# Kernel tuning notes

Hardware: AMD Instinct MI355X
Metric: run time of the kernel (lower is better)

Reference implementation:

```python
import jax, jax.numpy as jnp
import numpy as np

N, E, D, CAT, BINS, B, NNEG = 50000, 1600000, 128, 768, 100, 4096, 4


def _spmm(row, col, val, x):
    # torch.spmm(adj, x) with adj in COO form: out[r] += val * x[c]
    return jax.ops.segment_sum(val[:, None] * x[col], row, num_segments=N)


def _bn(x, g, b):
    # BatchNorm1d in training mode: biased batch statistics
    m = jnp.mean(x, axis=0)
    v = jnp.var(x, axis=0)
    return (x - m) * jax.lax.rsqrt(v + 1e-5) * g + b


def _two_att(qx, x, Wq1, bq1, Wk1, bk1, Wv1, bv1, Wq2, bq2, Wk2, bk2, Wv2, bv2, Wcat, bcat):
    # qx, x: [b, 2, D]. NOTE: original uses nn.Softmax(dim=1), i.e. softmax over the
    # QUERY axis of the [b, q, k] score matrix -- reproduced faithfully here.
    scale = 1.0 / (D ** 0.5)
    q = qx @ Wq1 + bq1
    k = x @ Wk1 + bk1
    v = x @ Wv1 + bv1
    a = jax.nn.softmax(jnp.einsum('bqd,bkd->bqk', q, k) * scale, axis=1)
    h = jnp.einsum('bqk,bkd->bqd', a, v)
    q = h @ Wq2 + bq2
    k = h @ Wk2 + bk2
    v = h @ Wv2 + bv2
    a = jax.nn.softmax(jnp.einsum('bqd,bkd->bqk', q, k) * scale, axis=1)
    h = jnp.einsum('bqk,bkd->bqd', a, v)
    return jnp.concatenate([h[:, 0], h[:, 1]], axis=1) @ Wcat + bcat


def setup_inputs():
    key = jax.random.key(0)
    ks = jax.random.split(key, 32)
    p = lambda i, shape: jax.random.normal(ks[i], shape, dtype=jnp.float32) * 0.05
    return {
        'features': jax.random.normal(ks[0], (N, 2 * CAT), dtype=jnp.float32),
        'price': jax.random.randint(ks[1], (N,), 0, BINS),
        'adj_row': jax.random.randint(ks[2], (E,), 0, N),
        'adj_col': jax.random.randint(ks[3], (E,), 0, N),
        'adj_val': jax.random.uniform(ks[4], (E,), dtype=jnp.float32),
        'train_set': jax.random.randint(ks[5], (B, 2 + NNEG), 0, N),
        'W_cid2': p(6, (CAT, D)), 'b_cid2': p(7, (D,)),
        'W_cid3': p(8, (CAT, D)), 'b_cid3': p(9, (D,)),
        'price_table': p(10, (BINS, D)),
        'W_emb': p(11, (3 * D, D)), 'b_emb': p(12, (D,)),
        'W_low': p(13, (D, D)), 'W_mid': p(14, (D, D)),
        'bn1_g': jnp.ones((D,), jnp.float32), 'bn1_b': jnp.zeros((D,), jnp.float32),
        'bn2_g': jnp.ones((D,), jnp.float32), 'bn2_b': jnp.zeros((D,), jnp.float32),
        'Wq1': p(15, (D, D)), 'bq1': p(16, (D,)),
        'Wk1': p(17, (D, D)), 'bk1': p(18, (D,)),
        'Wv1': p(19, (D, D)), 'bv1': p(20, (D,)),
        'Wq2': p(21, (D, D)), 'bq2': p(22, (D,)),
        'Wk2': p(23, (D, D)), 'bk2': p(24, (D,)),
        'Wv2': p(25, (D, D)), 'bv2': p(26, (D,)),
        'Wcat': p(27, (2 * D, D)), 'bcat': p(28, (D,)),
    }


def reference(features, price, adj_row, adj_col, adj_val, train_set,
              W_cid2, b_cid2, W_cid3, b_cid3, price_table, W_emb, b_emb,
              W_low, W_mid, bn1_g, bn1_b, bn2_g, bn2_b,
              Wq1, bq1, Wk1, bk1, Wv1, bv1, Wq2, bq2, Wk2, bk2, Wv2, bv2, Wcat, bcat):
    # item embedding
    e2 = features[:, :CAT] @ W_cid2 + b_cid2
    e3 = features[:, CAT:] @ W_cid3 + b_cid3
    ep = price_table[price]
    item = jax.nn.relu(jnp.concatenate([e2, e3, ep], axis=1) @ W_emb + b_emb)  # [N, D]
    # graph convolutions (low / mid frequency)
    ag = _spmm(adj_row, adj_col, adj_val, item)
    low = (0.5 * ag + 0.5 * item) @ W_low
    mid = (0.5 * _spmm(adj_row, adj_col, adj_val, ag) - 0.5 * item) @ W_mid
    out = jnp.stack([_bn(low, bn1_g, bn1_b), _bn(mid, bn2_g, bn2_b)], axis=1)  # [N, 2, D]
    # gather triples
    key_e = out[train_set[:, 0]]   # [B, 2, D]
    pos_e = out[train_set[:, 1]]   # [B, 2, D]
    neg_e = out[train_set[:, 2:]]  # [B, NNEG, 2, D]
    ap = (Wq1, bq1, Wk1, bk1, Wv1, bv1, Wq2, bq2, Wk2, bk2, Wv2, bv2, Wcat, bcat)
    klp = _two_att(pos_e, key_e, *ap)  # [B, D]
    pl = _two_att(key_e, pos_e, *ap)   # [B, D]
    # vectorize the per-negative loop by folding NNEG into batch
    Bn = key_e.shape[0]
    key_rep = jnp.broadcast_to(key_e[:, None], (Bn, NNEG, 2, D)).reshape(Bn * NNEG, 2, D)
    neg_flat = neg_e.reshape(Bn * NNEG, 2, D)
    kln = _two_att(neg_flat, key_rep, *ap).reshape(Bn, NNEG, D)
    nl = _two_att(key_rep, neg_flat, *ap).reshape(Bn, NNEG, D)
    pos_scores = jnp.sum(klp * pl, axis=1)        # [B]
    neg_scores = jnp.sum(kln * nl, axis=2)        # [B, NNEG]
    return -jnp.mean(jnp.log(jax.nn.sigmoid(pos_scores[:, None] - neg_scores) + 1e-9))
```

## Files before the change

### kernel.cpp

```cpp
#include <hip/hip_runtime.h>
#include <hip/hip_bf16.h>


typedef __attribute__((ext_vector_type(4))) float  f32x4;
typedef __attribute__((ext_vector_type(2))) float  f32x2;
typedef __attribute__((ext_vector_type(8))) short  s16x8;
typedef __attribute__((ext_vector_type(4))) short  s16x4;
typedef __attribute__((ext_vector_type(8))) __bf16 bf16x8;

#define NN   50000
#define EE   1600000
#define BQ   4096
#define NNEG 4

__device__ __forceinline__ short f2b(float x) {
    union { float f; unsigned u; } c; c.f = x;
    unsigned r = c.u + 0x7FFF + ((c.u >> 16) & 1);
    return (short)(r >> 16);
}
__device__ __forceinline__ float blo(unsigned u) { return __builtin_bit_cast(float, u << 16); }
__device__ __forceinline__ float bhi(unsigned u) { return __builtin_bit_cast(float, u & 0xffff0000u); }
__device__ __forceinline__ unsigned pk2(float a, float b) {
    return (unsigned)(unsigned short)f2b(a) | ((unsigned)(unsigned short)f2b(b) << 16);
}

template<bool TWOSRC, bool PRICE, bool RELU, bool OUTBF>
__global__ __launch_bounds__(256)
void gemm_bf16(const float* __restrict__ A1, const float* __restrict__ A2,
               float alpha, float beta,
               const short* __restrict__ WT, const float* __restrict__ bias,
               const int* __restrict__ price, const float* __restrict__ ptab,
               float* __restrict__ Y, unsigned short* __restrict__ Yb,
               int ldY, int rows, int K)
{
    __shared__ short Alds[128][32];
    __shared__ short Wlds[128][32];

    const int t    = threadIdx.x;
    const int lane = t & 63;
    const int w    = t >> 6;
    const int r0   = blockIdx.x * 128;
    const int c0   = blockIdx.y * 128;
    const short* WTb = WT + (size_t)c0 * K;

    f32x4 acc[4][4];
#pragma unroll
    for (int m = 0; m < 4; ++m)
#pragma unroll
        for (int n = 0; n < 4; ++n) acc[m][n] = (f32x4)0.f;

    const int srow = t >> 3;
    const int skk  = (t & 7) * 4;
    const int wn   = t >> 1;
    const int wkp  = (t & 1) * 16;

    const int wr   = (w >> 1) * 64;
    const int wc   = (w & 1) * 64;
    const int rsel = lane & 15;
    const int kb   = (lane >> 4) * 8;

    for (int k0 = 0; k0 < K; k0 += 32) {
#pragma unroll
        for (int i = 0; i < 4; ++i) {
            int r  = srow + i * 32;
            int rg = r0 + r; rg = rg < rows ? rg : rows - 1;
            float4 va = *(const float4*)(A1 + (size_t)rg * K + (k0 + skk));
            if (TWOSRC) {
                float4 vb = *(const float4*)(A2 + (size_t)rg * K + (k0 + skk));
                va.x = alpha * va.x + beta * vb.x;
                va.y = alpha * va.y + beta * vb.y;
                va.z = alpha * va.z + beta * vb.z;
                va.w = alpha * va.w + beta * vb.w;
            }
            s16x4 sv; sv[0]=f2b(va.x); sv[1]=f2b(va.y); sv[2]=f2b(va.z); sv[3]=f2b(va.w);
            int sw = ((r >> 1) & 3) * 8;
            *(s16x4*)&Alds[r][skk ^ sw] = sv;
        }
        {
            const short* p = WTb + (size_t)wn * K + (k0 + wkp);
            s16x8 w0 = *(const s16x8*)p;
            s16x8 w1 = *(const s16x8*)(p + 8);
            int sw = ((wn >> 1) & 3) * 8;
            *(s16x8*)&Wlds[wn][wkp ^ sw]       = w0;
            *(s16x8*)&Wlds[wn][(wkp + 8) ^ sw] = w1;
        }
        __syncthreads();

        s16x8 af[4], bfr[4];
#pragma unroll
        for (int m = 0; m < 4; ++m) {
            int r = wr + m * 16 + rsel;
            af[m] = *(const s16x8*)&Alds[r][kb ^ (((r >> 1) & 3) * 8)];
        }
#pragma unroll
        for (int n = 0; n < 4; ++n) {
            int r = wc + n * 16 + rsel;
            bfr[n] = *(const s16x8*)&Wlds[r][kb ^ (((r >> 1) & 3) * 8)];
        }
#pragma unroll
        for (int m = 0; m < 4; ++m)
#pragma unroll
            for (int n = 0; n < 4; ++n)
                acc[m][n] = __builtin_amdgcn_mfma_f32_16x16x32_bf16(
                    __builtin_bit_cast(bf16x8, af[m]),
                    __builtin_bit_cast(bf16x8, bfr[n]), acc[m][n], 0, 0, 0);
        __syncthreads();
    }

    const int crow = (lane >> 4) * 4;
#pragma unroll
    for (int m = 0; m < 4; ++m) {
        int rbase = r0 + wr + m * 16 + crow;
#pragma unroll
        for (int i = 0; i < 4; ++i) {
            int gr = rbase + i;
            bool ok = (gr < rows);
            int pidx = 0;
            if (PRICE) pidx = ok ? price[gr] : 0;
#pragma unroll
            for (int n = 0; n < 4; ++n) {
                int coll = wc + n * 16 + rsel;
                int cc   = c0 + coll;
                float v  = acc[m][n][i];
                if (bias)  v += bias[cc];
                if (PRICE) v += ptab[pidx * 128 + coll];
                if (RELU)  v = fmaxf(v, 0.f);
                if (ok) {
                    Y[(size_t)gr * ldY + cc] = v;
                    if (OUTBF) Yb[(size_t)gr * ldY + cc] = (unsigned short)f2b(v);
                }
            }
        }
    }
}

template<bool OUTBF>
__global__ __launch_bounds__(256)
void gemm_a16(const unsigned short* __restrict__ A,
              const short* __restrict__ WT, const float* __restrict__ bias,
              float* __restrict__ Y, unsigned short* __restrict__ Yb,
              int ldY, int rows, int K)
{
    __shared__ short Alds[128][32];
    __shared__ short Wlds[128][32];

    const int t    = threadIdx.x;
    const int lane = t & 63;
    const int w    = t >> 6;
    const int r0   = blockIdx.x * 128;
    const int c0   = blockIdx.y * 128;
    const short* WTb = WT + (size_t)c0 * K;

    f32x4 acc[4][4];
#pragma unroll
    for (int m = 0; m < 4; ++m)
#pragma unroll
        for (int n = 0; n < 4; ++n) acc[m][n] = (f32x4)0.f;

    const int srow = t >> 1;
    const int skk  = (t & 1) * 16;
    const int wn   = t >> 1;
    const int wkp  = (t & 1) * 16;

    const int wr   = (w >> 1) * 64;
    const int wc   = (w & 1) * 64;
    const int rsel = lane & 15;
    const int kb   = (lane >> 4) * 8;

    for (int k0 = 0; k0 < K; k0 += 32) {
        {
            int rg = r0 + srow; rg = rg < rows ? rg : rows - 1;
            const unsigned short* p = A + (size_t)rg * K + (k0 + skk);
            s16x8 a0 = *(const s16x8*)p;
            s16x8 a1 = *(const s16x8*)(p + 8);
            int sw = ((srow >> 1) & 3) * 8;
            *(s16x8*)&Alds[srow][skk ^ sw]       = a0;
            *(s16x8*)&Alds[srow][(skk + 8) ^ sw] = a1;
        }
        {
            const short* p = WTb + (size_t)wn * K + (k0 + wkp);
            s16x8 w0 = *(const s16x8*)p;
            s16x8 w1 = *(const s16x8*)(p + 8);
            int sw = ((wn >> 1) & 3) * 8;
            *(s16x8*)&Wlds[wn][wkp ^ sw]       = w0;
            *(s16x8*)&Wlds[wn][(wkp + 8) ^ sw] = w1;
        }
        __syncthreads();

        s16x8 af[4], bfr[4];
#pragma unroll
        for (int m = 0; m < 4; ++m) {
            int r = wr + m * 16 + rsel;
            af[m] = *(const s16x8*)&Alds[r][kb ^ (((r >> 1) & 3) * 8)];
        }
#pragma unroll
        for (int n = 0; n < 4; ++n) {
            int r = wc + n * 16 + rsel;
            bfr[n] = *(const s16x8*)&Wlds[r][kb ^ (((r >> 1) & 3) * 8)];
        }
#pragma unroll
        for (int m = 0; m < 4; ++m)
#pragma unroll
            for (int n = 0; n < 4; ++n)
                acc[m][n] = __builtin_amdgcn_mfma_f32_16x16x32_bf16(
                    __builtin_bit_cast(bf16x8, af[m]),
                    __builtin_bit_cast(bf16x8, bfr[n]), acc[m][n], 0, 0, 0);
        __syncthreads();
    }

    const int crow = (lane >> 4) * 4;
#pragma unroll
    for (int m = 0; m < 4; ++m) {
        int rbase = r0 + wr + m * 16 + crow;
#pragma unroll
        for (int i = 0; i < 4; ++i) {
            int gr = rbase + i;
            bool ok = (gr < rows);
#pragma unroll
            for (int n = 0; n < 4; ++n) {
                int cc = c0 + wc + n * 16 + rsel;
                float v = acc[m][n][i];
                if (bias) v += bias[cc];
                if (ok) {
                    if (OUTBF) Yb[(size_t)gr * ldY + cc] = (unsigned short)f2b(v);
                    else       Y [(size_t)gr * ldY + cc] = v;
                }
            }
        }
    }
}

__global__ __launch_bounds__(256)
void hist_rows(const int* __restrict__ row, int* __restrict__ cnt)
{
    int e = blockIdx.x * 256 + threadIdx.x;
    if (e < EE) atomicAdd(&cnt[row[e]], 1);
}

__global__ __launch_bounds__(1024)
void scan_a(const int* __restrict__ cnt, int* __restrict__ rp, int* __restrict__ bsum)
{
    __shared__ int tmp[1024];
    int t = threadIdx.x, g = blockIdx.x * 1024 + t;
    int v = (g < NN) ? cnt[g] : 0;
    tmp[t] = v;
    __syncthreads();
    for (int off = 1; off < 1024; off <<= 1) {
        int a = (t >= off) ? tmp[t - off] : 0;
        __syncthreads();
        tmp[t] += a;
        __syncthreads();
    }
    if (g < NN) rp[g] = tmp[t] - v;
    if (t == 1023) bsum[blockIdx.x] = tmp[t];
}

__global__ __launch_bounds__(64)
void scan_b(int* __restrict__ bsum, int nb)
{
    int lane = threadIdx.x;
    int orig = (lane < nb) ? bsum[lane] : 0;
    int v = orig;
    for (int off = 1; off < 64; off <<= 1) {
        int u = __shfl_up(v, off);
        if (lane >= off) v += u;
    }
    if (lane < nb) bsum[lane] = v - orig;
}

__global__ __launch_bounds__(1024)
void scan_c(int* __restrict__ rp, int* __restrict__ cur, const int* __restrict__ bsum)
{
    int t = threadIdx.x, g = blockIdx.x * 1024 + t;
    if (g < NN) {
        int v = rp[g] + bsum[blockIdx.x];
        rp[g] = v; cur[g] = v;
    }
    if (g == 0) rp[NN] = EE;
}

__global__ __launch_bounds__(256)
void scatter_edges(const int* __restrict__ row, const int* __restrict__ col,
                   const float* __restrict__ val, int* __restrict__ cur,
                   int2* __restrict__ pedge)
{
    int e = blockIdx.x * 256 + threadIdx.x;
    if (e >= EE) return;
    int p = atomicAdd(&cur[row[e]], 1);
    pedge[p] = make_int2(col[e], __float_as_int(val[e]));
}

template<bool WRITEB>
__global__ __launch_bounds__(256)
void spmm_csr(const int* __restrict__ rp, const int2* __restrict__ pedge,
              const unsigned short* __restrict__ xb,
              float* __restrict__ y, unsigned short* __restrict__ yb)
{
    int w    = (blockIdx.x * 256 + threadIdx.x) >> 6;
    int lane = threadIdx.x & 63;
    if (w >= NN) return;
    int s = rp[w], e = rp[w + 1];
    int d = lane * 2;
    float ax = 0.f, ay = 0.f;
    int i = s;
    for (; i + 4 <= e; i += 4) {
        int2 e0 = pedge[i], e1 = pedge[i+1], e2 = pedge[i+2], e3 = pedge[i+3];
        unsigned x0 = *(const unsigned*)(xb + (size_t)e0.x * 128 + d);
        unsigned x1 = *(const unsigned*)(xb + (size_t)e1.x * 128 + d);
        unsigned x2 = *(const unsigned*)(xb + (size_t)e2.x * 128 + d);
        unsigned x3 = *(const unsigned*)(xb + (size_t)e3.x * 128 + d);
        float v0 = __builtin_bit_cast(float, e0.y);
        float v1 = __builtin_bit_cast(float, e1.y);
        float v2 = __builtin_bit_cast(float, e2.y);
        float v3 = __builtin_bit_cast(float, e3.y);
        ax += v0 * blo(x0) + v1 * blo(x1) + v2 * blo(x2) + v3 * blo(x3);
        ay += v0 * bhi(x0) + v1 * bhi(x1) + v2 * bhi(x2) + v3 * bhi(x3);
    }
    for (; i < e; ++i) {
        int2 e0 = pedge[i];
        unsigned x0 = *(const unsigned*)(xb + (size_t)e0.x * 128 + d);
        float v0 = __builtin_bit_cast(float, e0.y);
        ax += v0 * blo(x0); ay += v0 * bhi(x0);
    }
    f32x2 r; r.x = ax; r.y = ay;
    *(f32x2*)(y + (size_t)w * 128 + d) = r;
    if (WRITEB) *(unsigned*)(yb + (size_t)w * 128 + d) = pk2(ax, ay);
}

__global__ __launch_bounds__(256)
void colstats(const float* __restrict__ low, const float* __restrict__ mid,
              float* __restrict__ stats, int nrows)
{
    const float* src = blockIdx.y ? mid : low;
    int c = threadIdx.x & 127;
    int h = threadIdx.x >> 7;
    int rs = blockIdx.x * 512;
    int re = min(rs + 512, nrows);
    float s1 = 0.f, s2 = 0.f;
    for (int r = rs + h; r < re; r += 2) {
        float xv = src[(size_t)r * 128 + c];
        s1 += xv; s2 += xv * xv;
    }
    __shared__ float l1[256], l2[256];
    l1[threadIdx.x] = s1; l2[threadIdx.x] = s2;
    __syncthreads();
    if (h == 0) {
        s1 = l1[c] + l1[128 + c];
        s2 = l2[c] + l2[128 + c];
        atomicAdd(&stats[blockIdx.y * 256 + c],       s1);
        atomicAdd(&stats[blockIdx.y * 256 + 128 + c], s2);
    }
}

__global__ __launch_bounds__(256)
void bn_scalebias(const float* __restrict__ stats,
                  const float* g1, const float* b1,
                  const float* g2, const float* b2,
                  float* __restrict__ sb, float inv_n)
{
    int t = threadIdx.x;
    int mat = t >> 7, c = t & 127;
    float mean = stats[mat * 256 + c] * inv_n;
    float var  = stats[mat * 256 + 128 + c] * inv_n - mean * mean;
    float s = (mat ? g2[c] : g1[c]) * rsqrtf(var + 1e-5f);
    float tt = (mat ? b2[c] : b1[c]) - mean * s;
    sb[mat * 256 + c] = s;
    sb[mat * 256 + 128 + c] = tt;
}

__global__ __launch_bounds__(256)
void gather_norm(const float* __restrict__ low, const float* __restrict__ mid,
                 const float* __restrict__ sb, const int* __restrict__ ts,
                 unsigned short* __restrict__ out)
{
    int idx = blockIdx.x * 256 + threadIdx.x;
    int c   = idx & 127;
    int seq = (idx >> 7) & 1;
    int r   = idx >> 8;
    int node;
    if      (r < 4096) node = ts[r * 6];
    else if (r < 8192) node = ts[(r - 4096) * 6 + 1];
    else { int rr = r - 8192; node = ts[(rr >> 2) * 6 + 2 + (rr & 3)]; }
    float xv = (seq ? mid : low)[(size_t)node * 128 + c];
    float yv = xv * sb[seq * 256 + c] + sb[seq * 256 + 128 + c];
    out[(size_t)r * 256 + seq * 128 + c] = (unsigned short)f2b(yv);
}

template<int LAYER>
__global__ __launch_bounds__(256)
void attn_fused(const unsigned short* __restrict__ qkv,
                unsigned short* __restrict__ h, int ntot)
{
    int gw   = (blockIdx.x * 256 + threadIdx.x) >> 6;
    int lane = threadIdx.x & 63;
    if (gw >= ntot) return;
    int qtok, ktok, orow;
    if (LAYER == 1) {
        if      (gw < 4096)  { int g = gw;         qtok = 8192  + g*2; ktok = g*2;          orow = g*2; }
        else if (gw < 8192)  { int g = gw - 4096;  qtok = g*2;         ktok = 8192 + g*2;   orow = 8192 + g*2; }
        else if (gw < 24576) { int g = gw - 8192;  qtok = 16384 + g*2; ktok = (g>>2)*2;     orow = 16384 + g*2; }
        else                 { int g = gw - 24576; qtok = (g>>2)*2;    ktok = 16384 + g*2;  orow = 49152 + g*2; }
    } else {
        qtok = gw * 2; ktok = gw * 2; orow = gw * 2;
    }
    int d = lane * 2;
    unsigned q0 = *(const unsigned*)(qkv + (size_t)qtok * 384 + d);
    unsigned q1 = *(const unsigned*)(qkv + (size_t)(qtok+1) * 384 + d);
    unsigned k0 = *(const unsigned*)(qkv + (size_t)ktok * 384 + 128 + d);
    unsigned k1 = *(const unsigned*)(qkv + (size_t)(ktok+1) * 384 + 128 + d);
    float s00 = blo(q0)*blo(k0) + bhi(q0)*bhi(k0);
    float s01 = blo(q0)*blo(k1) + bhi(q0)*bhi(k1);
    float s10 = blo(q1)*blo(k0) + bhi(q1)*bhi(k0);
    float s11 = blo(q1)*blo(k1) + bhi(q1)*bhi(k1);
#pragma unroll
    for (int off = 32; off; off >>= 1) {
        s00 += __shfl_xor(s00, off);
        s01 += __shfl_xor(s01, off);
        s10 += __shfl_xor(s10, off);
        s11 += __shfl_xor(s11, off);
    }
    const float scale = 0.08838834764831845f;
    s00 *= scale; s01 *= scale; s10 *= scale; s11 *= scale;
    float m0 = fmaxf(s00, s10), m1 = fmaxf(s01, s11);
    float e00 = __expf(s00 - m0), e10 = __expf(s10 - m0);
    float e01 = __expf(s01 - m1), e11 = __expf(s11 - m1);
    float i0 = 1.f / (e00 + e10), i1 = 1.f / (e01 + e11);
    float a00 = e00 * i0, a10 = e10 * i0;
    float a01 = e01 * i1, a11 = e11 * i1;
    unsigned v0 = *(const unsigned*)(qkv + (size_t)ktok * 384 + 256 + d);
    unsigned v1 = *(const unsigned*)(qkv + (size_t)(ktok+1) * 384 + 256 + d);
    float h0x = a00*blo(v0) + a01*blo(v1), h0y = a00*bhi(v0) + a01*bhi(v1);
    float h1x = a10*blo(v0) + a11*blo(v1), h1y = a10*bhi(v0) + a11*bhi(v1);
    *(unsigned*)(h + (size_t)orow * 128 + d)       = pk2(h0x, h0y);
    *(unsigned*)(h + (size_t)(orow + 1) * 128 + d) = pk2(h1x, h1y);
}

__global__ __launch_bounds__(256)
void scores_kernel(const float* __restrict__ cat, float* __restrict__ scores)
{
    int gw   = (blockIdx.x * 256 + threadIdx.x) >> 6;
    int lane = threadIdx.x & 63;
    if (gw >= 20480) return;
    const float *pa, *pb;
    if (gw < BQ) { pa = cat + (size_t)gw * 128;            pb = cat + (size_t)(BQ + gw) * 128; }
    else { int n = gw - BQ; pa = cat + (size_t)(2*BQ + n) * 128; pb = cat + (size_t)(2*BQ + BQ*NNEG + n) * 128; }
    f32x2 a = *(const f32x2*)(pa + lane * 2);
    f32x2 b = *(const f32x2*)(pb + lane * 2);
    float s = a.x * b.x + a.y * b.y;
#pragma unroll
    for (int off = 32; off; off >>= 1) s += __shfl_xor(s, off);
    if (lane == 0) scores[gw] = s;
}

__global__ __launch_bounds__(256)
void loss_kernel(const float* __restrict__ scores, float* __restrict__ out)
{
    int t = threadIdx.x;
    float acc = 0.f;
    for (int i = t; i < BQ * NNEG; i += 256) {
        int b = i >> 2;
        float x = scores[b] - scores[BQ + i];
        float sig = 1.f / (1.f + __expf(-x));
        acc += __logf(sig + 1e-9f);
    }
    __shared__ float red[256];
    red[t] = acc; __syncthreads();
    for (int s = 128; s > 0; s >>= 1) { if (t < s) red[t] += red[t + s]; __syncthreads(); }
    if (t == 0) out[0] = -red[0] / (float)(BQ * NNEG);
}

__global__ void pack_wc(const float* __restrict__ W2, const float* __restrict__ W3,
                        const float* __restrict__ We, short* __restrict__ WcT)
{
    int k = blockIdx.x, n = threadIdx.x;
    const float* Wrow = (k < 768) ? (W2 + (size_t)k * 128) : (W3 + (size_t)(k - 768) * 128);
    const float* Web  = We + ((k < 768) ? 0 : 128 * 128);
    float acc = 0.f;
    for (int j = 0; j < 128; ++j) acc += Wrow[j] * Web[j * 128 + n];
    WcT[(size_t)n * 1536 + k] = f2b(acc);
}

__global__ __launch_bounds__(128)
void pack_misc(const float* PT, const float* We,
               const float* b2, const float* b3, const float* bemb,
               const float* Wq1, const float* Wk1, const float* Wv1,
               const float* bq1, const float* bk1, const float* bv1,
               const float* Wq2, const float* Wk2, const float* Wv2,
               const float* bq2, const float* bk2, const float* bv2,
               const float* Wlow, const float* Wmid, const float* Wct,
               float* ptab2, float* bias_c,
               short* Wqkv1T, float* bqkv1,
               short* Wqkv2T, float* bqkv2,
               short* WlowT, short* WmidT, short* WcatT)
{
    int b = blockIdx.x, t = threadIdx.x;
    if (b < 100) {
        const float* Web = We + 256 * 128;
        float acc = 0.f;
        for (int j = 0; j < 128; ++j) acc += PT[b * 128 + j] * Web[j * 128 + t];
        ptab2[b * 128 + t] = acc;
    } else if (b == 100) {
        float acc = bemb[t];
        for (int j = 0; j < 128; ++j)
            acc += b2[j] * We[j * 128 + t] + b3[j] * We[(128 + j) * 128 + t];
        bias_c[t] = acc;
    } else if (b < 229) {
        int k = b - 101;
        Wqkv1T[(size_t)(      t) * 128 + k] = f2b(Wq1[k * 128 + t]);
        Wqkv1T[(size_t)(128 + t) * 128 + k] = f2b(Wk1[k * 128 + t]);
        Wqkv1T[(size_t)(256 + t) * 128 + k] = f2b(Wv1[k * 128 + t]);
        if (k == 0) { bqkv1[t] = bq1[t]; bqkv1[128 + t] = bk1[t]; bqkv1[256 + t] = bv1[t]; }
    } else if (b < 357) {
        int k = b - 229;
        Wqkv2T[(size_t)(      t) * 128 + k] = f2b(Wq2[k * 128 + t]);
        Wqkv2T[(size_t)(128 + t) * 128 + k] = f2b(Wk2[k * 128 + t]);
        Wqkv2T[(size_t)(256 + t) * 128 + k] = f2b(Wv2[k * 128 + t]);
        if (k == 0) { bqkv2[t] = bq2[t]; bqkv2[128 + t] = bk2[t]; bqkv2[256 + t] = bv2[t]; }
    } else if (b < 485) {
        int k = b - 357;
        WlowT[(size_t)t * 128 + k] = f2b(Wlow[k * 128 + t]);
    } else if (b < 613) {
        int k = b - 485;
        WmidT[(size_t)t * 128 + k] = f2b(Wmid[k * 128 + t]);
    } else {
        int k = b - 613;
        WcatT[(size_t)t * 256 + k] = f2b(Wct[k * 128 + t]);
    }
}

extern "C" void kernel_launch(void* const* d_in, const int* in_sizes, int n_in,
                              void* d_out, int out_size, void* d_ws, size_t ws_size,
                              hipStream_t stream)
{
    const float* features = (const float*)d_in[0];
    const int*   price    = (const int*)  d_in[1];
    const int*   adj_row  = (const int*)  d_in[2];
    const int*   adj_col  = (const int*)  d_in[3];
    const float* adj_val  = (const float*)d_in[4];
    const int*   train_set= (const int*)  d_in[5];
    const float* W_cid2   = (const float*)d_in[6];
    const float* b_cid2   = (const float*)d_in[7];
    const float* W_cid3   = (const float*)d_in[8];
    const float* b_cid3   = (const float*)d_in[9];
    const float* ptable   = (const float*)d_in[10];
    const float* W_emb    = (const float*)d_in[11];
    const float* b_emb    = (const float*)d_in[12];
    const float* W_low    = (const float*)d_in[13];
    const float* W_mid    = (const float*)d_in[14];
    const float* bn1_g    = (const float*)d_in[15];
    const float* bn1_b    = (const float*)d_in[16];
    const float* bn2_g    = (const float*)d_in[17];
    const float* bn2_b    = (const float*)d_in[18];
    const float* Wq1 = (const float*)d_in[19]; const float* bq1 = (const float*)d_in[20];
    const float* Wk1 = (const float*)d_in[21]; const float* bk1 = (const float*)d_in[22];
    const float* Wv1 = (const float*)d_in[23]; const float* bv1 = (const float*)d_in[24];
    const float* Wq2 = (const float*)d_in[25]; const float* bq2 = (const float*)d_in[26];
    const float* Wk2 = (const float*)d_in[27]; const float* bk2 = (const float*)d_in[28];
    const float* Wv2 = (const float*)d_in[29]; const float* bv2 = (const float*)d_in[30];
    const float* Wcat= (const float*)d_in[31]; const float* bcat= (const float*)d_in[32];

    float* ws = (float*)d_ws;

    const size_t SZ_NODE = (size_t)NN * 128;
    float*          item    = ws;
    float*          ag      = ws + 6400000;
    float*          ag2     = ws + 12800000;
    float*          low     = ws + 19200000;
    float*          mid     = ws + 25600000;
    unsigned short* item_bf = (unsigned short*)(ws + 32000000);
    unsigned short* ag_bf   = (unsigned short*)(ws + 35200000);
    unsigned short* gath_b  = (unsigned short*)(ws + 38400000);
    unsigned short* qkv1b   = (unsigned short*)(ws + 41545728);
    unsigned short* h1b     = (unsigned short*)(ws + 50982912);
    unsigned short* qkv2b   = (unsigned short*)(ws + 56225792);
    unsigned short* h2b     = (unsigned short*)(ws + 71954432);
    float*          cat     = ws + 77197312;
    int*            ibase   = (int*)(ws + 82440192);
    int*   rp    = ibase;
    int*   cur   = ibase + 50016;
    float* stats = (float*)(ibase + 100032);
    int*   bsum  = ibase + 100544;
    int2*  pedge = (int2*)(ibase + 100640);
    float* wb    = (float*)(ibase + 3300640);
    short* WcT    = (short*)wb;
    float* ptab2  = wb + 98304;
    float* bias_c = wb + 111104;
    short* Wqkv1T = (short*)(wb + 111232);
    float* bqkv1  = wb + 135808;
    short* Wqkv2T = (short*)(wb + 136192);
    float* bqkv2  = wb + 160768;
    short* WlowT  = (short*)(wb + 161152);
    short* WmidT  = (short*)(wb + 169344);
    short* WcatT  = (short*)(wb + 177536);
    float* sb     = wb + 193920;
    float* scores = wb + 194432;

    hipLaunchKernelGGL(pack_wc,   dim3(1536), dim3(128), 0, stream, W_cid2, W_cid3, W_emb, WcT);
    hipLaunchKernelGGL(pack_misc, dim3(869),  dim3(128), 0, stream,
                       ptable, W_emb, b_cid2, b_cid3, b_emb,
                       Wq1, Wk1, Wv1, bq1, bk1, bv1,
                       Wq2, Wk2, Wv2, bq2, bk2, bv2,
                       W_low, W_mid, Wcat,
                       ptab2, bias_c, Wqkv1T, bqkv1, Wqkv2T, bqkv2,
                       WlowT, WmidT, WcatT);

    hipMemsetAsync(cur, 0, (50016 + 512) * 4, stream);

    hipLaunchKernelGGL(hist_rows,     dim3(6250), dim3(256),  0, stream, adj_row, cur);
    hipLaunchKernelGGL(scan_a,        dim3(49),   dim3(1024), 0, stream, cur, rp, bsum);
    hipLaunchKernelGGL(scan_b,        dim3(1),    dim3(64),   0, stream, bsum, 49);
    hipLaunchKernelGGL(scan_c,        dim3(49),   dim3(1024), 0, stream, rp, cur, bsum);
    hipLaunchKernelGGL(scatter_edges, dim3(6250), dim3(256),  0, stream,
                       adj_row, adj_col, adj_val, cur, pedge);

    hipLaunchKernelGGL((gemm_bf16<false, true, true, true>), dim3(391, 1), dim3(256), 0, stream,
                       features, nullptr, 1.f, 0.f, WcT, bias_c, price, ptab2,
                       item, item_bf, 128, NN, 1536);

    hipLaunchKernelGGL((spmm_csr<true>), dim3(12500), dim3(256), 0, stream,
                       rp, pedge, item_bf, ag, ag_bf);
    hipLaunchKernelGGL((gemm_bf16<true, false, false, false>), dim3(391, 1), dim3(256), 0, stream,
                       ag, item, 0.5f, 0.5f, WlowT, nullptr, nullptr, nullptr,
                       low, nullptr, 128, NN, 128);

    hipLaunchKernelGGL((spmm_csr<false>), dim3(12500), dim3(256), 0, stream,
                       rp, pedge, ag_bf, ag2, nullptr);
    hipLaunchKernelGGL((gemm_bf16<true, false, false, false>), dim3(391, 1), dim3(256), 0, stream,
                       ag2, item, 0.5f, -0.5f, WmidT, nullptr, nullptr, nullptr,
                       mid, nullptr, 128, NN, 128);

    hipLaunchKernelGGL(colstats, dim3(98, 2), dim3(256), 0, stream, low, mid, stats, NN);
    hipLaunchKernelGGL(bn_scalebias, dim3(1), dim3(256), 0, stream,
                       stats, bn1_g, bn1_b, bn2_g, bn2_b, sb, 1.f / (float)NN);

    hipLaunchKernelGGL(gather_norm, dim3(24576), dim3(256), 0, stream,
                       low, mid, sb, train_set, gath_b);

    hipLaunchKernelGGL((gemm_a16<true>), dim3(384, 3), dim3(256), 0, stream,
                       gath_b, Wqkv1T, bqkv1, nullptr, qkv1b, 384, 49152, 128);

    hipLaunchKernelGGL((attn_fused<1>), dim3(10240), dim3(256), 0, stream, qkv1b, h1b, 40960);

    hipLaunchKernelGGL((gemm_a16<true>), dim3(640, 3), dim3(256), 0, stream,
                       h1b, Wqkv2T, bqkv2, nullptr, qkv2b, 384, 81920, 128);

    hipLaunchKernelGGL((attn_fused<2>), dim3(10240), dim3(256), 0, stream, qkv2b, h2b, 40960);

    hipLaunchKernelGGL((gemm_a16<false>), dim3(320, 1), dim3(256), 0, stream,
                       h2b, WcatT, bcat, cat, nullptr, 128, 40960, 256);

    hipLaunchKernelGGL(scores_kernel, dim3(5120), dim3(256), 0, stream, cat, scores);
    hipLaunchKernelGGL(loss_kernel, dim3(1), dim3(256), 0, stream, scores, (float*)d_out);
}
```

Baseline: 1.123 ms.

## Keep node intermediates in bf16 and fuse low/mid GEMMs with concatenated K

All node-level intermediates (item, ag, ag2, low, mid) are now stored only in bf16 rather than fp32 plus a bf16 copy. The 0.5 mixing is folded into stacked weight matrices, so the low and mid projections become one K=256 GEMM over [ag|item] and [ag2|item] launched together. The SpMM inner loop is unrolled to 8 edges to keep more gathers in flight, and colstats and gather_norm read packed bf16 pairs. The aim is to cut HBM traffic and launch count, at the cost of extra bf16 rounding in low/mid before the batch-norm statistics.

After: 1.047 ms. 6.8% less time.

```diff
diff --git a/kernel.cpp b/kernel.cpp
--- a/kernel.cpp
+++ b/kernel.cpp
@@ -24,14 +24,11 @@
     return (unsigned)(unsigned short)f2b(a) | ((unsigned)(unsigned short)f2b(b) << 16);
 }
 
-template<bool TWOSRC, bool PRICE, bool RELU, bool OUTBF>
-__global__ __launch_bounds__(256)
-void gemm_bf16(const float* __restrict__ A1, const float* __restrict__ A2,
-               float alpha, float beta,
+__global__ __launch_bounds__(256)
+void gemm_item(const float* __restrict__ A1,
                const short* __restrict__ WT, const float* __restrict__ bias,
                const int* __restrict__ price, const float* __restrict__ ptab,
-               float* __restrict__ Y, unsigned short* __restrict__ Yb,
-               int ldY, int rows, int K)
+               unsigned short* __restrict__ Yb, int rows, int K)
 {
     __shared__ short Alds[128][32];
     __shared__ short Wlds[128][32];
@@ -40,8 +37,6 @@
     const int lane = t & 63;
     const int w    = t >> 6;
     const int r0   = blockIdx.x * 128;
-    const int c0   = blockIdx.y * 128;
-    const short* WTb = WT + (size_t)c0 * K;
 
     f32x4 acc[4][4];
 #pragma unroll
@@ -65,19 +60,12 @@
             int r  = srow + i * 32;
             int rg = r0 + r; rg = rg < rows ? rg : rows - 1;
             float4 va = *(const float4*)(A1 + (size_t)rg * K + (k0 + skk));
-            if (TWOSRC) {
-                float4 vb = *(const float4*)(A2 + (size_t)rg * K + (k0 + skk));
-                va.x = alpha * va.x + beta * vb.x;
-                va.y = alpha * va.y + beta * vb.y;
-                va.z = alpha * va.z + beta * vb.z;
-                va.w = alpha * va.w + beta * vb.w;
-            }
             s16x4 sv; sv[0]=f2b(va.x); sv[1]=f2b(va.y); sv[2]=f2b(va.z); sv[3]=f2b(va.w);
             int sw = ((r >> 1) & 3) * 8;
             *(s16x4*)&Alds[r][skk ^ sw] = sv;
         }
         {
-            const short* p = WTb + (size_t)wn * K + (k0 + wkp);
+            const short* p = WT + (size_t)wn * K + (k0 + wkp);
             s16x8 w0 = *(const s16x8*)p;
             s16x8 w1 = *(const s16x8*)(p + 8);
             int sw = ((wn >> 1) & 3) * 8;
@@ -115,20 +103,109 @@
         for (int i = 0; i < 4; ++i) {
             int gr = rbase + i;
             bool ok = (gr < rows);
-            int pidx = 0;
-            if (PRICE) pidx = ok ? price[gr] : 0;
+            int pidx = ok ? price[gr] : 0;
 #pragma unroll
             for (int n = 0; n < 4; ++n) {
-                int coll = wc + n * 16 + rsel;
-                int cc   = c0 + coll;
-                float v  = acc[m][n][i];
-                if (bias)  v += bias[cc];
-                if (PRICE) v += ptab[pidx * 128 + coll];
-                if (RELU)  v = fmaxf(v, 0.f);
-                if (ok) {
-                    Y[(size_t)gr * ldY + cc] = v;
-                    if (OUTBF) Yb[(size_t)gr * ldY + cc] = (unsigned short)f2b(v);
-                }
+                int cc = wc + n * 16 + rsel;
+                float v = acc[m][n][i] + bias[cc] + ptab[pidx * 128 + cc];
+                v = fmaxf(v, 0.f);
+                if (ok) Yb[(size_t)gr * 128 + cc] = (unsigned short)f2b(v);
+            }
+        }
+    }
+}
+
+__global__ __launch_bounds__(256)
+void gemm_lowmid(const unsigned short* __restrict__ ag_bf,
+                 const unsigned short* __restrict__ ag2_bf,
+                 const unsigned short* __restrict__ item_bf,
+                 const short* __restrict__ WlowT2, const short* __restrict__ WmidT2,
+                 unsigned short* __restrict__ low_bf, unsigned short* __restrict__ mid_bf,
+                 int rows)
+{
+    __shared__ short Alds[128][32];
+    __shared__ short Wlds[128][32];
+
+    const unsigned short* A0 = blockIdx.y ? ag2_bf : ag_bf;
+    const short*          WT = blockIdx.y ? WmidT2 : WlowT2;
+    unsigned short*       Yb = blockIdx.y ? mid_bf : low_bf;
+
+    const int t    = threadIdx.x;
+    const int lane = t & 63;
+    const int w    = t >> 6;
+    const int r0   = blockIdx.x * 128;
+
+    f32x4 acc[4][4];
+#pragma unroll
+    for (int m = 0; m < 4; ++m)
+#pragma unroll
+        for (int n = 0; n < 4; ++n) acc[m][n] = (f32x4)0.f;
+
+    const int srow = t >> 1;
+    const int skk  = (t & 1) * 16;
+    const int wn   = t >> 1;
+    const int wkp  = (t & 1) * 16;
+
+    const int wr   = (w >> 1) * 64;
+    const int wc   = (w & 1) * 64;
+    const int rsel = lane & 15;
+    const int kb   = (lane >> 4) * 8;
+
+    for (int k0 = 0; k0 < 256; k0 += 32) {
+        {
+            int rg = r0 + srow; rg = rg < rows ? rg : rows - 1;
+            const unsigned short* tab = (k0 < 128) ? A0 : item_bf;
+            int kc = (k0 + skk) & 127;
+            const unsigned short* p = tab + (size_t)rg * 128 + kc;
+            s16x8 a0 = *(const s16x8*)p;
+            s16x8 a1 = *(const s16x8*)(p + 8);
+            int sw = ((srow >> 1) & 3) * 8;
+            *(s16x8*)&Alds[srow][skk ^ sw]       = a0;
+            *(s16x8*)&Alds[srow][(skk + 8) ^ sw] = a1;
+        }
+        {
+            const short* p = WT + (size_t)wn * 256 + (k0 + wkp);
+            s16x8 w0 = *(const s16x8*)p;
+            s16x8 w1 = *(const s16x8*)(p + 8);
+            int sw = ((wn >> 1) & 3) * 8;
+            *(s16x8*)&Wlds[wn][wkp ^ sw]       = w0;
+            *(s16x8*)&Wlds[wn][(wkp + 8) ^ sw] = w1;
+        }
+        __syncthreads();
+
+        s16x8 af[4], bfr[4];
+#pragma unroll
+        for (int m = 0; m < 4; ++m) {
+            int r = wr + m * 16 + rsel;
+            af[m] = *(const s16x8*)&Alds[r][kb ^ (((r >> 1) & 3) * 8)];
+        }
+#pragma unroll
+        for (int n = 0; n < 4; ++n) {
+            int r = wc + n * 16 + rsel;
+            bfr[n] = *(const s16x8*)&Wlds[r][kb ^ (((r >> 1) & 3) * 8)];
+        }
+#pragma unroll
+        for (int m = 0; m < 4; ++m)
+#pragma unroll
+            for (int n = 0; n < 4; ++n)
+                acc[m][n] = __builtin_amdgcn_mfma_f32_16x16x32_bf16(
+                    __builtin_bit_cast(bf16x8, af[m]),
+                    __builtin_bit_cast(bf16x8, bfr[n]), acc[m][n], 0, 0, 0);
+        __syncthreads();
+    }
+
+    const int crow = (lane >> 4) * 4;
+#pragma unroll
+    for (int m = 0; m < 4; ++m) {
+        int rbase = r0 + wr + m * 16 + crow;
+#pragma unroll
+        for (int i = 0; i < 4; ++i) {
+            int gr = rbase + i;
+            if (gr >= rows) continue;
+#pragma unroll
+            for (int n = 0; n < 4; ++n) {
+                int cc = wc + n * 16 + rsel;
+                Yb[(size_t)gr * 128 + cc] = (unsigned short)f2b(acc[m][n][i]);
             }
         }
     }
@@ -290,11 +367,10 @@
     pedge[p] = make_int2(col[e], __float_as_int(val[e]));
 }
 
-template<bool WRITEB>
 __global__ __launch_bounds__(256)
 void spmm_csr(const int* __restrict__ rp, const int2* __restrict__ pedge,
               const unsigned short* __restrict__ xb,
-              float* __restrict__ y, unsigned short* __restrict__ yb)
+              unsigned short* __restrict__ yb)
 {
     int w    = (blockIdx.x * 256 + threadIdx.x) >> 6;
     int lane = threadIdx.x & 63;
@@ -303,18 +379,19 @@
     int d = lane * 2;
     float ax = 0.f, ay = 0.f;
     int i = s;
-    for (; i + 4 <= e; i += 4) {
-        int2 e0 = pedge[i], e1 = pedge[i+1], e2 = pedge[i+2], e3 = pedge[i+3];
-        unsigned x0 = *(const unsigned*)(xb + (size_t)e0.x * 128 + d);
-        unsigned x1 = *(const unsigned*)(xb + (size_t)e1.x * 128 + d);
-        unsigned x2 = *(const unsigned*)(xb + (size_t)e2.x * 128 + d);
-        unsigned x3 = *(const unsigned*)(xb + (size_t)e3.x * 128 + d);
-        float v0 = __builtin_bit_cast(float, e0.y);
-        float v1 = __builtin_bit_cast(float, e1.y);
-        float v2 = __builtin_bit_cast(float, e2.y);
-        float v3 = __builtin_bit_cast(float, e3.y);
-        ax += v0 * blo(x0) + v1 * blo(x1) + v2 * blo(x2) + v3 * blo(x3);
-        ay += v0 * bhi(x0) + v1 * bhi(x1) + v2 * bhi(x2) + v3 * bhi(x3);
+    for (; i + 8 <= e; i += 8) {
+        int2 ed[8]; unsigned xv[8];
+#pragma unroll
+        for (int j = 0; j < 8; ++j) ed[j] = pedge[i + j];
+#pragma unroll
+        for (int j = 0; j < 8; ++j)
+            xv[j] = *(const unsigned*)(xb + (size_t)ed[j].x * 128 + d);
+#pragma unroll
+        for (int j = 0; j < 8; ++j) {
+            float v = __builtin_bit_cast(float, ed[j].y);
+            ax += v * blo(xv[j]);
+            ay += v * bhi(xv[j]);
+        }
     }
     for (; i < e; ++i) {
         int2 e0 = pedge[i];
@@ -322,33 +399,40 @@
         float v0 = __builtin_bit_cast(float, e0.y);
         ax += v0 * blo(x0); ay += v0 * bhi(x0);
     }
-    f32x2 r; r.x = ax; r.y = ay;
-    *(f32x2*)(y + (size_t)w * 128 + d) = r;
-    if (WRITEB) *(unsigned*)(yb + (size_t)w * 128 + d) = pk2(ax, ay);
-}
-
-__global__ __launch_bounds__(256)
-void colstats(const float* __restrict__ low, const float* __restrict__ mid,
+    *(unsigned*)(yb + (size_t)w * 128 + d) = pk2(ax, ay);
+}
+
+__global__ __launch_bounds__(256)
+void colstats(const unsigned short* __restrict__ low,
+              const unsigned short* __restrict__ mid,
               float* __restrict__ stats, int nrows)
 {
-    const float* src = blockIdx.y ? mid : low;
-    int c = threadIdx.x & 127;
-    int h = threadIdx.x >> 7;
+    const unsigned* src = (const unsigned*)(blockIdx.y ? mid : low);
+    int p = threadIdx.x & 63;
+    int h = threadIdx.x >> 6;
     int rs = blockIdx.x * 512;
     int re = min(rs + 512, nrows);
-    float s1 = 0.f, s2 = 0.f;
-    for (int r = rs + h; r < re; r += 2) {
-        float xv = src[(size_t)r * 128 + c];
-        s1 += xv; s2 += xv * xv;
-    }
-    __shared__ float l1[256], l2[256];
-    l1[threadIdx.x] = s1; l2[threadIdx.x] = s2;
+    float s1a = 0.f, s2a = 0.f, s1b = 0.f, s2b = 0.f;
+    for (int r = rs + h; r < re; r += 4) {
+        unsigned u = src[(size_t)r * 64 + p];
+        float a = blo(u), b = bhi(u);
+        s1a += a; s2a += a * a;
+        s1b += b; s2b += b * b;
+    }
+    __shared__ float4 red[256];
+    red[threadIdx.x] = make_float4(s1a, s2a, s1b, s2b);
     __syncthreads();
     if (h == 0) {
-        s1 = l1[c] + l1[128 + c];
-        s2 = l2[c] + l2[128 + c];
-        atomicAdd(&stats[blockIdx.y * 256 + c],       s1);
-        atomicAdd(&stats[blockIdx.y * 256 + 128 + c], s2);
+        float4 v0 = red[p], v1 = red[64 + p], v2 = red[128 + p], v3 = red[192 + p];
+        float t1a = v0.x + v1.x + v2.x + v3.x;
+        float t2a = v0.y + v1.y + v2.y + v3.y;
+        float t1b = v0.z + v1.z + v2.z + v3.z;
+        float t2b = v0.w + v1.w + v2.w + v3.w;
+        int base = blockIdx.y * 256;
+        atomicAdd(&stats[base + 2 * p],           t1a);
+        atomicAdd(&stats[base + 2 * p + 1],       t1b);
+        atomicAdd(&stats[base + 128 + 2 * p],     t2a);
+        atomicAdd(&stats[base + 128 + 2 * p + 1], t2b);
     }
 }
 
@@ -369,21 +453,25 @@
 }
 
 __global__ __launch_bounds__(256)
-void gather_norm(const float* __restrict__ low, const float* __restrict__ mid,
+void gather_norm(const unsigned short* __restrict__ low,
+                 const unsigned short* __restrict__ mid,
                  const float* __restrict__ sb, const int* __restrict__ ts,
                  unsigned short* __restrict__ out)
 {
     int idx = blockIdx.x * 256 + threadIdx.x;
-    int c   = idx & 127;
-    int seq = (idx >> 7) & 1;
-    int r   = idx >> 8;
+    int p   = idx & 63;
+    int seq = (idx >> 6) & 1;
+    int r   = idx >> 7;
     int node;
     if      (r < 4096) node = ts[r * 6];
     else if (r < 8192) node = ts[(r - 4096) * 6 + 1];
     else { int rr = r - 8192; node = ts[(rr >> 2) * 6 + 2 + (rr & 3)]; }
-    float xv = (seq ? mid : low)[(size_t)node * 128 + c];
-    float yv = xv * sb[seq * 256 + c] + sb[seq * 256 + 128 + c];
-    out[(size_t)r * 256 + seq * 128 + c] = (unsigned short)f2b(yv);
+    const unsigned* src = (const unsigned*)(seq ? mid : low);
+    unsigned u = src[(size_t)node * 64 + p];
+    int c0 = 2 * p, c1 = 2 * p + 1;
+    float ya = blo(u) * sb[seq * 256 + c0] + sb[seq * 256 + 128 + c0];
+    float yb = bhi(u) * sb[seq * 256 + c1] + sb[seq * 256 + 128 + c1];
+    ((unsigned*)out)[(size_t)r * 128 + seq * 64 + p] = pk2(ya, yb);
 }
 
 template<int LAYER>
@@ -491,7 +579,7 @@
                float* ptab2, float* bias_c,
                short* Wqkv1T, float* bqkv1,
                short* Wqkv2T, float* bqkv2,
-               short* WlowT, short* WmidT, short* WcatT)
+               short* WlowT2, short* WmidT2, short* WcatT)
 {
     int b = blockIdx.x, t = threadIdx.x;
     if (b < 100) {
@@ -518,10 +606,13 @@
         if (k == 0) { bqkv2[t] = bq2[t]; bqkv2[128 + t] = bk2[t]; bqkv2[256 + t] = bv2[t]; }
     } else if (b < 485) {
         int k = b - 357;
-        WlowT[(size_t)t * 128 + k] = f2b(Wlow[k * 128 + t]);
+        short v = f2b(0.5f * Wlow[k * 128 + t]);
+        WlowT2[(size_t)t * 256 + k]       = v;
+        WlowT2[(size_t)t * 256 + 128 + k] = v;
     } else if (b < 613) {
         int k = b - 485;
-        WmidT[(size_t)t * 128 + k] = f2b(Wmid[k * 128 + t]);
+        WmidT2[(size_t)t * 256 + k]       = f2b( 0.5f * Wmid[k * 128 + t]);
+        WmidT2[(size_t)t * 256 + 128 + k] = f2b(-0.5f * Wmid[k * 128 + t]);
     } else {
         int k = b - 613;
         WcatT[(size_t)t * 256 + k] = f2b(Wct[k * 128 + t]);
@@ -561,21 +652,18 @@
 
     float* ws = (float*)d_ws;
 
-    const size_t SZ_NODE = (size_t)NN * 128;
-    float*          item    = ws;
-    float*          ag      = ws + 6400000;
-    float*          ag2     = ws + 12800000;
-    float*          low     = ws + 19200000;
-    float*          mid     = ws + 25600000;
-    unsigned short* item_bf = (unsigned short*)(ws + 32000000);
-    unsigned short* ag_bf   = (unsigned short*)(ws + 35200000);
-    unsigned short* gath_b  = (unsigned short*)(ws + 38400000);
-    unsigned short* qkv1b   = (unsigned short*)(ws + 41545728);
-    unsigned short* h1b     = (unsigned short*)(ws + 50982912);
-    unsigned short* qkv2b   = (unsigned short*)(ws + 56225792);
-    unsigned short* h2b     = (unsigned short*)(ws + 71954432);
-    float*          cat     = ws + 77197312;
-    int*            ibase   = (int*)(ws + 82440192);
+    unsigned short* item_bf = (unsigned short*)(ws);
+    unsigned short* ag_bf   = (unsigned short*)(ws + 3200000);
+    unsigned short* ag2_bf  = (unsigned short*)(ws + 6400000);
+    unsigned short* low_bf  = (unsigned short*)(ws + 9600000);
+    unsigned short* mid_bf  = (unsigned short*)(ws + 12800000);
+    unsigned short* gath_b  = (unsigned short*)(ws + 16000000);
+    unsigned short* qkv1b   = (unsigned short*)(ws + 19145728);
+    unsigned short* h1b     = (unsigned short*)(ws + 28582912);
+    unsigned short* qkv2b   = (unsigned short*)(ws + 33825792);
+    unsigned short* h2b     = (unsigned short*)(ws + 49554432);
+    float*          cat     = ws + 54797312;
+    int*            ibase   = (int*)(ws + 60040192);
     int*   rp    = ibase;
     int*   cur   = ibase + 50016;
     float* stats = (float*)(ibase + 100032);
@@ -589,11 +677,11 @@
     float* bqkv1  = wb + 135808;
     short* Wqkv2T = (short*)(wb + 136192);
     float* bqkv2  = wb + 160768;
-    short* WlowT  = (short*)(wb + 161152);
-    short* WmidT  = (short*)(wb + 169344);
-    short* WcatT  = (short*)(wb + 177536);
-    float* sb     = wb + 193920;
-    float* scores = wb + 194432;
+    short* WlowT2 = (short*)(wb + 161152);
+    short* WmidT2 = (short*)(wb + 177536);
+    short* WcatT  = (short*)(wb + 193920);
+    float* sb     = wb + 210304;
+    float* scores = wb + 210816;
 
     hipLaunchKernelGGL(pack_wc,   dim3(1536), dim3(128), 0, stream, W_cid2, W_cid3, W_emb, WcT);
     hipLaunchKernelGGL(pack_misc, dim3(869),  dim3(128), 0, stream,
@@ -602,7 +690,7 @@
                        Wq2, Wk2, Wv2, bq2, bk2, bv2,
                        W_low, W_mid, Wcat,
                        ptab2, bias_c, Wqkv1T, bqkv1, Wqkv2T, bqkv2,
-                       WlowT, WmidT, WcatT);
+                       WlowT2, WmidT2, WcatT);
 
     hipMemsetAsync(cur, 0, (50016 + 512) * 4, stream);
 
@@ -613,28 +701,21 @@
     hipLaunchKernelGGL(scatter_edges, dim3(6250), dim3(256),  0, stream,
                        adj_row, adj_col, adj_val, cur, pedge);
 
-    hipLaunchKernelGGL((gemm_bf16<false, true, true, true>), dim3(391, 1), dim3(256), 0, stream,
-                       features, nullptr, 1.f, 0.f, WcT, bias_c, price, ptab2,
-                       item, item_bf, 128, NN, 1536);
-
-    hipLaunchKernelGGL((spmm_csr<true>), dim3(12500), dim3(256), 0, stream,
-                       rp, pedge, item_bf, ag, ag_bf);
-    hipLaunchKernelGGL((gemm_bf16<true, false, false, false>), dim3(391, 1), dim3(256), 0, stream,
-                       ag, item, 0.5f, 0.5f, WlowT, nullptr, nullptr, nullptr,
-                       low, nullptr, 128, NN, 128);
-
-    hipLaunchKernelGGL((spmm_csr<false>), dim3(12500), dim3(256), 0, stream,
-                       rp, pedge, ag_bf, ag2, nullptr);
-    hipLaunchKernelGGL((gemm_bf16<true, false, false, false>), dim3(391, 1), dim3(256), 0, stream,
-                       ag2, item, 0.5f, -0.5f, WmidT, nullptr, nullptr, nullptr,
-                       mid, nullptr, 128, NN, 128);
-
-    hipLaunchKernelGGL(colstats, dim3(98, 2), dim3(256), 0, stream, low, mid, stats, NN);
+    hipLaunchKernelGGL(gemm_item, dim3(391), dim3(256), 0, stream,
+                       features, WcT, bias_c, price, ptab2, item_bf, NN, 1536);
+
+    hipLaunchKernelGGL(spmm_csr, dim3(12500), dim3(256), 0, stream, rp, pedge, item_bf, ag_bf);
+    hipLaunchKernelGGL(spmm_csr, dim3(12500), dim3(256), 0, stream, rp, pedge, ag_bf, ag2_bf);
+
+    hipLaunchKernelGGL(gemm_lowmid, dim3(391, 2), dim3(256), 0, stream,
+                       ag_bf, ag2_bf, item_bf, WlowT2, WmidT2, low_bf, mid_bf, NN);
+
+    hipLaunchKernelGGL(colstats, dim3(98, 2), dim3(256), 0, stream, low_bf, mid_bf, stats, NN);
     hipLaunchKernelGGL(bn_scalebias, dim3(1), dim3(256), 0, stream,
                        stats, bn1_g, bn1_b, bn2_g, bn2_b, sb, 1.f / (float)NN);
 
-    hipLaunchKernelGGL(gather_norm, dim3(24576), dim3(256), 0, stream,
-                       low, mid, sb, train_set, gath_b);
+    hipLaunchKernelGGL(gather_norm, dim3(12288), dim3(256), 0, stream,
+                       low_bf, mid_bf, sb, train_set, gath_b);
 
     hipLaunchKernelGGL((gemm_a16<true>), dim3(384, 3), dim3(256), 0, stream,
                        gath_b, Wqkv1T, bqkv1, nullptr, qkv1b, 384, 49152, 128);
```
